# Kernel tuning notes

Measured on AMD Instinct MI355X. Metric: run time of the kernel, lower is better.

## Reference

```python
import jax, jax.numpy as jnp
import numpy as np

B, N_IN, N_OUT, K, V = 8, 2048, 2048, 64, 64


def setup_inputs() -> dict:
    key = jax.random.key(0)
    k1, k2, k3 = jax.random.split(key, 3)
    return {
        "key": jax.random.normal(k1, (B, N_IN, 1, K), dtype=jnp.float32),
        "query": jax.random.normal(k2, (B, 1, N_OUT, K), dtype=jnp.float32),
        "value": jax.random.normal(k3, (B, N_IN, V), dtype=jnp.float32),
    }


def reference(key, query, value):
    ks = key.shape[-1]
    # sum(key * query, 3) / sqrt(key_size)  ==  batched GEMM over key_size
    # weights: [B, n_inputs, n_outputs]
    weights = jnp.einsum("bik,bok->bio", key[:, :, 0, :], query[:, 0, :, :]) / jnp.sqrt(
        jnp.asarray(ks, dtype=key.dtype)
    )
    weights = jax.nn.softmax(weights, axis=1)  # softmax over n_inputs
    # sum(weights[...,None] * value[:,:,None,:], 1) -> [B, n_outputs, value_size]
    vals = jnp.einsum("bio,biv->bov", weights, value)
    # row-wise L2 normalize each [value_size] vector
    vals = vals / (jnp.linalg.norm(vals, axis=-1, keepdims=True) + 1e-12)
    values = jnp.swapaxes(vals, 1, 2)  # [B, value_size, n_outputs]
    return values, weights
```

## Files before the change

### kernel.cpp

```cpp
#include <hip/hip_runtime.h>

#define NB 8
#define NN 2048
#define KK 64
#define VV 64
#define OS 32
#define NT 32
#define SCALE 0.18033688011112043f
#define USTRIDE 36

typedef __bf16 bfrag __attribute__((ext_vector_type(8)));
typedef float  f32x4 __attribute__((ext_vector_type(4)));

__device__ __forceinline__ int swz(int row, int colByte) {
  return row * 128 + (colByte ^ ((row & 7) << 4));
}

__device__ __forceinline__ bfrag lds_frag(const unsigned short* base, int row, int colByte) {
  return *reinterpret_cast<const bfrag*>(reinterpret_cast<const char*>(base) + swz(row, colByte));
}

__device__ __forceinline__ bfrag g_frag(const float* __restrict__ g) {
  const float4* p = reinterpret_cast<const float4*>(g);
  float4 x = p[0], y = p[1];
  bfrag r;
  r[0] = (__bf16)x.x; r[1] = (__bf16)x.y; r[2] = (__bf16)x.z; r[3] = (__bf16)x.w;
  r[4] = (__bf16)y.x; r[5] = (__bf16)y.y; r[6] = (__bf16)y.z; r[7] = (__bf16)y.w;
  return r;
}

struct KS { float4 f[4]; };
__device__ __forceinline__ void k_load(KS& s, const float* __restrict__ g) {
  const float4* p = reinterpret_cast<const float4*>(g);
  s.f[0] = p[0]; s.f[1] = p[1]; s.f[2] = p[2]; s.f[3] = p[3];
}
__device__ __forceinline__ void k_write(const KS& s, unsigned short* lds, int row, int colByte) {
  const float* f = reinterpret_cast<const float*>(&s.f[0]);
  bfrag a, b;
#pragma unroll
  for (int j = 0; j < 8; ++j) a[j] = (__bf16)f[j];
#pragma unroll
  for (int j = 0; j < 8; ++j) b[j] = (__bf16)f[8 + j];
  *reinterpret_cast<bfrag*>(reinterpret_cast<char*>(lds) + swz(row, colByte)) = a;
  *reinterpret_cast<bfrag*>(reinterpret_cast<char*>(lds) + swz(row, colByte + 16)) = b;
}

struct VS { float4 f[4]; };
__device__ __forceinline__ void v_load(VS& s, const float* __restrict__ g) {
  const float4* p = reinterpret_cast<const float4*>(g);
  s.f[0] = p[0]; s.f[1] = p[1];
  const float4* q = reinterpret_cast<const float4*>(g + VV);
  s.f[2] = q[0]; s.f[3] = q[1];
}
__device__ __forceinline__ void v_write(const VS& s, unsigned short* lds, int il, int v0) {
  const float* lo = reinterpret_cast<const float*>(&s.f[0]);
  const float* hi = reinterpret_cast<const float*>(&s.f[2]);
#pragma unroll
  for (int j = 0; j < 8; ++j) {
    __bf16 two[2] = { (__bf16)lo[j], (__bf16)hi[j] };
    *reinterpret_cast<unsigned*>(reinterpret_cast<char*>(lds) + swz(v0 + j, il * 2)) =
        *reinterpret_cast<unsigned*>(two);
  }
}

__global__ void __launch_bounds__(512, 4) attn_fused(
    const float* __restrict__ key, const float* __restrict__ query,
    const float* __restrict__ value, float* __restrict__ out)
{
  __shared__ __align__(16) char smem[32768];
  __shared__ float Red[4][16];
  __shared__ float InvD[OS];
  __shared__ float Nn[OS];
  unsigned short* Kt0 = reinterpret_cast<unsigned short*>(smem);
  unsigned short* Kt1 = reinterpret_cast<unsigned short*>(smem + 8192);
  unsigned short* Vt0 = reinterpret_cast<unsigned short*>(smem + 16384);
  unsigned short* Vt1 = reinterpret_cast<unsigned short*>(smem + 24576);
  float* U0 = reinterpret_cast<float*>(smem);
  float* U1 = reinterpret_cast<float*>(smem + 9216);

  const int tid  = threadIdx.x;
  const int lane = tid & 63;
  const int w    = tid >> 6;
  const int l15  = lane & 15;
  const int l4   = lane >> 4;
  const int vhalf = w & 1;
  const int ihalf = (w >> 1) & 1;
  const int oh    = w >> 2;

  const int b  = blockIdx.x & 7;
  const int o0 = (blockIdx.x >> 3) * OS;

  const float* Kg = key   + (size_t)b * NN * KK;
  const float* Qg = query + (size_t)b * NN * KK;
  const float* Vg = value + (size_t)b * NN * VV;
  float* outV = out + (size_t)b * VV * NN;
  float* outW = out + (size_t)NB * VV * NN + (size_t)b * NN * NN;

  bfrag qb0, qb1;
  {
    const float* qr = Qg + (size_t)(o0 + oh * 16 + l15) * KK;
    qb0 = g_frag(qr + l4 * 8);
    qb1 = g_frag(qr + 32 + l4 * 8);
  }

  const int krow = tid >> 2;
  const int kel  = (tid & 3) * 16;
  const int kcb  = (tid & 3) * 32;
  const int t2   = tid & 255;
  const int vil  = (t2 & 31) * 2;
  const int vv0  = (t2 >> 5) * 8;

  KS ks; VS vs;
  if (tid < 256) { k_load(ks, Kg + (size_t)krow * KK + kel); }
  else           { v_load(vs, Vg + (size_t)vil * VV + vv0); }
  if (tid < 256) k_write(ks, Kt0, krow, kcb);
  else           v_write(vs, Vt0, vil, vv0);
  __syncthreads();

  const int ip = (l15 & 3) + ((l15 >> 2) * 8);

  f32x4 uacc[2];
  { f32x4 z = {0.f,0.f,0.f,0.f}; uacc[0] = z; uacc[1] = z; }
  float Dacc = 0.f;

  for (int t = 0; t < NT; ++t) {
    unsigned short* Kc = (t & 1) ? Kt1 : Kt0;
    unsigned short* Vc = (t & 1) ? Vt1 : Vt0;
    unsigned short* Kn = (t & 1) ? Kt0 : Kt1;
    unsigned short* Vn = (t & 1) ? Vt0 : Vt1;
    if (t + 1 < NT) {
      if (tid < 256) k_load(ks, Kg + (size_t)((t + 1) * 64 + krow) * KK + kel);
      else           v_load(vs, Vg + (size_t)((t + 1) * 64 + vil) * VV + vv0);
    }
    const int r1 = ihalf * 32 + ip;
    bfrag ka10 = lds_frag(Kc, r1,     l4 * 16);
    bfrag ka11 = lds_frag(Kc, r1,     64 + l4 * 16);
    bfrag ka20 = lds_frag(Kc, r1 + 4, l4 * 16);
    bfrag ka21 = lds_frag(Kc, r1 + 4, 64 + l4 * 16);
    f32x4 z1 = {0.f,0.f,0.f,0.f}, z2 = {0.f,0.f,0.f,0.f};
    z1 = __builtin_amdgcn_mfma_f32_16x16x32_bf16(ka10, qb0, z1, 0, 0, 0);
    z1 = __builtin_amdgcn_mfma_f32_16x16x32_bf16(ka11, qb1, z1, 0, 0, 0);
    z2 = __builtin_amdgcn_mfma_f32_16x16x32_bf16(ka20, qb0, z2, 0, 0, 0);
    z2 = __builtin_amdgcn_mfma_f32_16x16x32_bf16(ka21, qb1, z2, 0, 0, 0);
    f32x4 e1, e2;
#pragma unroll
    for (int r = 0; r < 4; ++r) e1[r] = exp2f(z1[r] * SCALE);
#pragma unroll
    for (int r = 0; r < 4; ++r) e2[r] = exp2f(z2[r] * SCALE);
    Dacc += e1[0] + e1[1] + e1[2] + e1[3] + e2[0] + e2[1] + e2[2] + e2[3];
    bfrag eb;
#pragma unroll
    for (int r = 0; r < 4; ++r) eb[r]     = (__bf16)e1[r];
#pragma unroll
    for (int r = 0; r < 4; ++r) eb[4 + r] = (__bf16)e2[r];
#pragma unroll
    for (int vg = 0; vg < 2; ++vg) {
      bfrag va = lds_frag(Vc, vhalf * 32 + vg * 16 + l15, ihalf * 64 + l4 * 16);
      uacc[vg] = __builtin_amdgcn_mfma_f32_16x16x32_bf16(va, eb, uacc[vg], 0, 0, 0);
    }
    if (t + 1 < NT) {
      if (tid < 256) k_write(ks, Kn, krow, kcb);
      else           v_write(vs, Vn, vil, vv0);
    }
    __syncthreads();
  }

  {
    float d = Dacc;
    d += __shfl_xor(d, 16, 64);
    d += __shfl_xor(d, 32, 64);
    if ((w & 1) == 0 && lane < 16) Red[w >> 1][lane] = d;
  }
  {
    float* Ur = ihalf ? U1 : U0;
#pragma unroll
    for (int vg = 0; vg < 2; ++vg)
#pragma unroll
      for (int r = 0; r < 4; ++r)
        Ur[(vhalf * 32 + vg * 16 + l4 * 4 + r) * USTRIDE + oh * 16 + l15] = uacc[vg][r];
  }
  __syncthreads();
  {
    const int v = tid >> 3, o = (tid & 7) * 4;
    f32x4 a = *reinterpret_cast<f32x4*>(&U0[v * USTRIDE + o]);
    f32x4 c = *reinterpret_cast<f32x4*>(&U1[v * USTRIDE + o]);
    a = a + c;
    *reinterpret_cast<f32x4*>(&U0[v * USTRIDE + o]) = a;
  }
  __syncthreads();
  if (tid < OS) {
    float ssq = 0.f;
#pragma unroll
    for (int v = 0; v < VV; ++v) { float x = U0[v * USTRIDE + tid]; ssq += x * x; }
    Nn[tid] = 1.f / (sqrtf(ssq) + 1e-12f);
  } else if (tid < 2 * OS) {
    const int o = tid - OS, ohh = o >> 4;
    InvD[o] = 1.f / (Red[ohh * 2][o & 15] + Red[ohh * 2 + 1][o & 15]);
  }
  __syncthreads();
  {
    const int v = tid >> 3, o = (tid & 7) * 4;
    f32x4 a  = *reinterpret_cast<f32x4*>(&U0[v * USTRIDE + o]);
    f32x4 nn = *reinterpret_cast<f32x4*>(&Nn[o]);
    f32x4 r;
#pragma unroll
    for (int j = 0; j < 4; ++j) r[j] = a[j] * nn[j];
    *reinterpret_cast<f32x4*>(&outV[(size_t)v * NN + o0 + o]) = r;
  }
  f32x4 id = *reinterpret_cast<f32x4*>(&InvD[oh * 16 + l4 * 4]);
  __syncthreads();

  const int iq    = w & 3;
  const int kbrow = tid >> 3;
  const int kseg  = tid & 7;
  {
    const float4* kp = reinterpret_cast<const float4*>(Kg + (size_t)kbrow * KK + kseg * 8);
    float4 p0 = kp[0], p1 = kp[1];
    bfrag f;
    f[0] = (__bf16)p0.x; f[1] = (__bf16)p0.y; f[2] = (__bf16)p0.z; f[3] = (__bf16)p0.w;
    f[4] = (__bf16)p1.x; f[5] = (__bf16)p1.y; f[6] = (__bf16)p1.z; f[7] = (__bf16)p1.w;
    *reinterpret_cast<bfrag*>(reinterpret_cast<char*>(Kt0) + swz(kbrow, kseg * 16)) = f;
  }
  __syncthreads();
  for (int t = 0; t < NT; ++t) {
    unsigned short* Kc = (t & 1) ? Kt1 : Kt0;
    unsigned short* Kn = (t & 1) ? Kt0 : Kt1;
    float4 p0, p1;
    if (t + 1 < NT) {
      const float4* kp = reinterpret_cast<const float4*>(
          Kg + (size_t)((t + 1) * 64 + kbrow) * KK + kseg * 8);
      p0 = kp[0]; p1 = kp[1];
    }
    bfrag kb0 = lds_frag(Kc, iq * 16 + l15, l4 * 16);
    bfrag kb1 = lds_frag(Kc, iq * 16 + l15, 64 + l4 * 16);
    f32x4 z = {0.f,0.f,0.f,0.f};
    z = __builtin_amdgcn_mfma_f32_16x16x32_bf16(qb0, kb0, z, 0, 0, 0);
    z = __builtin_amdgcn_mfma_f32_16x16x32_bf16(qb1, kb1, z, 0, 0, 0);
    f32x4 ww;
#pragma unroll
    for (int r = 0; r < 4; ++r) ww[r] = exp2f(z[r] * SCALE) * id[r];
    float* wp = outW + (size_t)(t * 64 + iq * 16 + l15) * NN + o0 + oh * 16 + l4 * 4;
    *reinterpret_cast<f32x4*>(wp) = ww;
    if (t + 1 < NT) {
      bfrag f;
      f[0] = (__bf16)p0.x; f[1] = (__bf16)p0.y; f[2] = (__bf16)p0.z; f[3] = (__bf16)p0.w;
      f[4] = (__bf16)p1.x; f[5] = (__bf16)p1.y; f[6] = (__bf16)p1.z; f[7] = (__bf16)p1.w;
      *reinterpret_cast<bfrag*>(reinterpret_cast<char*>(Kn) + swz(kbrow, kseg * 16)) = f;
    }
    __syncthreads();
  }
}

extern "C" void kernel_launch(void* const* d_in, const int* in_sizes, int n_in,
                              void* d_out, int out_size, void* d_ws, size_t ws_size,
                              hipStream_t stream) {
  (void)in_sizes; (void)n_in; (void)d_ws; (void)ws_size; (void)out_size;
  const float* key   = (const float*)d_in[0];
  const float* query = (const float*)d_in[1];
  const float* value = (const float*)d_in[2];
  float* out = (float*)d_out;
  attn_fused<<<dim3(NB * (NN / OS)), dim3(512), 0, stream>>>(key, query, value, out);
}
```

Baseline: 78.70 us.

## Double output tile to 64 columns with 1024-thread blocks and direct-global K in weight pass

Each block now covers 64 output columns with 16 waves and streams 128 input rows per step, which halves the number of blocks and halves the redundant K/V reloads. The final weight-writing pass now reads K fragments straight from global memory, with no LDS staging or barriers, and each wave produces two 16-column groups. The cross-wave reductions are reworked into a serialized accumulation over four waves and a partial sum-of-squares for the norm. This raises LDS use to 64KB per block and the register load per thread, which may reduce occupancy, and the global K reads in the final pass are less coalesced.

```diff
diff --git a/kernel.cpp b/kernel.cpp
--- a/kernel.cpp
+++ b/kernel.cpp
@@ -4,20 +4,30 @@
 #define NN 2048
 #define KK 64
 #define VV 64
-#define OS 32
-#define NT 32
+#define OS 64
+#define ITEP 128
+#define NTA (NN / ITEP)
 #define SCALE 0.18033688011112043f
-#define USTRIDE 36
+#define UST 68
 
 typedef __bf16 bfrag __attribute__((ext_vector_type(8)));
 typedef float  f32x4 __attribute__((ext_vector_type(4)));
 
-__device__ __forceinline__ int swz(int row, int colByte) {
-  return row * 128 + (colByte ^ ((row & 7) << 4));
-}
-
-__device__ __forceinline__ bfrag lds_frag(const unsigned short* base, int row, int colByte) {
-  return *reinterpret_cast<const bfrag*>(reinterpret_cast<const char*>(base) + swz(row, colByte));
+__device__ __forceinline__ int swzK(int row, int colByte) {
+  const int key = ((row & 3) << 1) | ((row >> 3) & 1);
+  return row * 128 + (colByte ^ (key << 4));
+}
+__device__ __forceinline__ int swzV(int row, int colByte) {
+  return row * 256 + (colByte ^ ((row & 7) << 4));
+}
+
+__device__ __forceinline__ bfrag kfrag(const unsigned short* base, int row, int colByte) {
+  return *reinterpret_cast<const bfrag*>(
+      reinterpret_cast<const char*>(base) + swzK(row, colByte));
+}
+__device__ __forceinline__ bfrag vfrag(const unsigned short* base, int row, int colByte) {
+  return *reinterpret_cast<const bfrag*>(
+      reinterpret_cast<const char*>(base) + swzV(row, colByte));
 }
 
 __device__ __forceinline__ bfrag g_frag(const float* __restrict__ g) {
@@ -41,8 +51,8 @@
   for (int j = 0; j < 8; ++j) a[j] = (__bf16)f[j];
 #pragma unroll
   for (int j = 0; j < 8; ++j) b[j] = (__bf16)f[8 + j];
-  *reinterpret_cast<bfrag*>(reinterpret_cast<char*>(lds) + swz(row, colByte)) = a;
-  *reinterpret_cast<bfrag*>(reinterpret_cast<char*>(lds) + swz(row, colByte + 16)) = b;
+  *reinterpret_cast<bfrag*>(reinterpret_cast<char*>(lds) + swzK(row, colByte)) = a;
+  *reinterpret_cast<bfrag*>(reinterpret_cast<char*>(lds) + swzK(row, colByte + 16)) = b;
 }
 
 struct VS { float4 f[4]; };
@@ -58,34 +68,33 @@
 #pragma unroll
   for (int j = 0; j < 8; ++j) {
     __bf16 two[2] = { (__bf16)lo[j], (__bf16)hi[j] };
-    *reinterpret_cast<unsigned*>(reinterpret_cast<char*>(lds) + swz(v0 + j, il * 2)) =
+    *reinterpret_cast<unsigned*>(reinterpret_cast<char*>(lds) + swzV(v0 + j, il * 2)) =
         *reinterpret_cast<unsigned*>(two);
   }
 }
 
-__global__ void __launch_bounds__(512, 4) attn_fused(
+__global__ void __launch_bounds__(1024, 4) attn_fused(
     const float* __restrict__ key, const float* __restrict__ query,
     const float* __restrict__ value, float* __restrict__ out)
 {
-  __shared__ __align__(16) char smem[32768];
-  __shared__ float Red[4][16];
+  __shared__ __align__(16) char smem[65536];
+  __shared__ float Red[16][16];
   __shared__ float InvD[OS];
   __shared__ float Nn[OS];
   unsigned short* Kt0 = reinterpret_cast<unsigned short*>(smem);
-  unsigned short* Kt1 = reinterpret_cast<unsigned short*>(smem + 8192);
-  unsigned short* Vt0 = reinterpret_cast<unsigned short*>(smem + 16384);
-  unsigned short* Vt1 = reinterpret_cast<unsigned short*>(smem + 24576);
-  float* U0 = reinterpret_cast<float*>(smem);
-  float* U1 = reinterpret_cast<float*>(smem + 9216);
+  unsigned short* Kt1 = reinterpret_cast<unsigned short*>(smem + 16384);
+  unsigned short* Vt0 = reinterpret_cast<unsigned short*>(smem + 32768);
+  unsigned short* Vt1 = reinterpret_cast<unsigned short*>(smem + 49152);
+  float* Ured = reinterpret_cast<float*>(smem);
+  float* R2   = reinterpret_cast<float*>(smem + 20480);
 
   const int tid  = threadIdx.x;
   const int lane = tid & 63;
   const int w    = tid >> 6;
   const int l15  = lane & 15;
   const int l4   = lane >> 4;
-  const int vhalf = w & 1;
-  const int ihalf = (w >> 1) & 1;
-  const int oh    = w >> 2;
+  const int oh   = w >> 2;
+  const int iq   = w & 3;
 
   const int b  = blockIdx.x & 7;
   const int o0 = (blockIdx.x >> 3) * OS;
@@ -106,37 +115,39 @@
   const int krow = tid >> 2;
   const int kel  = (tid & 3) * 16;
   const int kcb  = (tid & 3) * 32;
-  const int t2   = tid & 255;
-  const int vil  = (t2 & 31) * 2;
-  const int vv0  = (t2 >> 5) * 8;
+  const int t2   = tid - 512;
+  const int vil  = (t2 & 63) * 2;
+  const int vg8  = (t2 >> 6) & 7;
+  const int vv0  = vg8 * 8;
 
   KS ks; VS vs;
-  if (tid < 256) { k_load(ks, Kg + (size_t)krow * KK + kel); }
+  if (tid < 512) { k_load(ks, Kg + (size_t)krow * KK + kel); }
   else           { v_load(vs, Vg + (size_t)vil * VV + vv0); }
-  if (tid < 256) k_write(ks, Kt0, krow, kcb);
+  if (tid < 512) k_write(ks, Kt0, krow, kcb);
   else           v_write(vs, Vt0, vil, vv0);
   __syncthreads();
 
   const int ip = (l15 & 3) + ((l15 >> 2) * 8);
 
-  f32x4 uacc[2];
-  { f32x4 z = {0.f,0.f,0.f,0.f}; uacc[0] = z; uacc[1] = z; }
+  f32x4 uacc[4];
+#pragma unroll
+  for (int vg = 0; vg < 4; ++vg) { f32x4 z = {0.f,0.f,0.f,0.f}; uacc[vg] = z; }
   float Dacc = 0.f;
 
-  for (int t = 0; t < NT; ++t) {
+  for (int t = 0; t < NTA; ++t) {
     unsigned short* Kc = (t & 1) ? Kt1 : Kt0;
     unsigned short* Vc = (t & 1) ? Vt1 : Vt0;
     unsigned short* Kn = (t & 1) ? Kt0 : Kt1;
     unsigned short* Vn = (t & 1) ? Vt0 : Vt1;
-    if (t + 1 < NT) {
-      if (tid < 256) k_load(ks, Kg + (size_t)((t + 1) * 64 + krow) * KK + kel);
-      else           v_load(vs, Vg + (size_t)((t + 1) * 64 + vil) * VV + vv0);
-    }
-    const int r1 = ihalf * 32 + ip;
-    bfrag ka10 = lds_frag(Kc, r1,     l4 * 16);
-    bfrag ka11 = lds_frag(Kc, r1,     64 + l4 * 16);
-    bfrag ka20 = lds_frag(Kc, r1 + 4, l4 * 16);
-    bfrag ka21 = lds_frag(Kc, r1 + 4, 64 + l4 * 16);
+    if (t + 1 < NTA) {
+      if (tid < 512) k_load(ks, Kg + (size_t)((t + 1) * ITEP + krow) * KK + kel);
+      else           v_load(vs, Vg + (size_t)((t + 1) * ITEP + vil) * VV + vv0);
+    }
+    const int r1 = iq * 32 + ip;
+    bfrag ka10 = kfrag(Kc, r1,     l4 * 16);
+    bfrag ka11 = kfrag(Kc, r1,     64 + l4 * 16);
+    bfrag ka20 = kfrag(Kc, r1 + 4, l4 * 16);
+    bfrag ka21 = kfrag(Kc, r1 + 4, 64 + l4 * 16);
     f32x4 z1 = {0.f,0.f,0.f,0.f}, z2 = {0.f,0.f,0.f,0.f};
     z1 = __builtin_amdgcn_mfma_f32_16x16x32_bf16(ka10, qb0, z1, 0, 0, 0);
     z1 = __builtin_amdgcn_mfma_f32_16x16x32_bf16(ka11, qb1, z1, 0, 0, 0);
@@ -154,12 +165,12 @@
 #pragma unroll
     for (int r = 0; r < 4; ++r) eb[4 + r] = (__bf16)e2[r];
 #pragma unroll
-    for (int vg = 0; vg < 2; ++vg) {
-      bfrag va = lds_frag(Vc, vhalf * 32 + vg * 16 + l15, ihalf * 64 + l4 * 16);
+    for (int vg = 0; vg < 4; ++vg) {
+      bfrag va = vfrag(Vc, vg * 16 + l15, iq * 64 + l4 * 16);
       uacc[vg] = __builtin_amdgcn_mfma_f32_16x16x32_bf16(va, eb, uacc[vg], 0, 0, 0);
     }
-    if (t + 1 < NT) {
-      if (tid < 256) k_write(ks, Kn, krow, kcb);
+    if (t + 1 < NTA) {
+      if (tid < 512) k_write(ks, Kn, krow, kcb);
       else           v_write(vs, Vn, vil, vv0);
     }
     __syncthreads();
@@ -169,85 +180,83 @@
     float d = Dacc;
     d += __shfl_xor(d, 16, 64);
     d += __shfl_xor(d, 32, 64);
-    if ((w & 1) == 0 && lane < 16) Red[w >> 1][lane] = d;
-  }
-  {
-    float* Ur = ihalf ? U1 : U0;
-#pragma unroll
-    for (int vg = 0; vg < 2; ++vg)
-#pragma unroll
-      for (int r = 0; r < 4; ++r)
-        Ur[(vhalf * 32 + vg * 16 + l4 * 4 + r) * USTRIDE + oh * 16 + l15] = uacc[vg][r];
-  }
-  __syncthreads();
-  {
-    const int v = tid >> 3, o = (tid & 7) * 4;
-    f32x4 a = *reinterpret_cast<f32x4*>(&U0[v * USTRIDE + o]);
-    f32x4 c = *reinterpret_cast<f32x4*>(&U1[v * USTRIDE + o]);
-    a = a + c;
-    *reinterpret_cast<f32x4*>(&U0[v * USTRIDE + o]) = a;
+    if (lane < 16) Red[w][lane] = d;
+  }
+#pragma unroll
+  for (int q = 0; q < 4; ++q) {
+    if (iq == q) {
+#pragma unroll
+      for (int vg = 0; vg < 4; ++vg)
+#pragma unroll
+        for (int r = 0; r < 4; ++r) {
+          const int idx = (vg * 16 + l4 * 4 + r) * UST + oh * 16 + l15;
+          if (q == 0) Ured[idx] = uacc[vg][r];
+          else        Ured[idx] += uacc[vg][r];
+        }
+    }
+    __syncthreads();
+  }
+  {
+    const int vgr = tid >> 6;
+    const int o   = tid & 63;
+    float s = 0.f;
+#pragma unroll
+    for (int j = 0; j < 4; ++j) {
+      float x = Ured[(vgr * 4 + j) * UST + o];
+      s += x * x;
+    }
+    R2[vgr * 64 + o] = s;
   }
   __syncthreads();
   if (tid < OS) {
-    float ssq = 0.f;
-#pragma unroll
-    for (int v = 0; v < VV; ++v) { float x = U0[v * USTRIDE + tid]; ssq += x * x; }
-    Nn[tid] = 1.f / (sqrtf(ssq) + 1e-12f);
+    float n = 0.f;
+#pragma unroll
+    for (int g = 0; g < 16; ++g) n += R2[g * 64 + tid];
+    Nn[tid] = 1.f / (sqrtf(n) + 1e-12f);
   } else if (tid < 2 * OS) {
-    const int o = tid - OS, ohh = o >> 4;
-    InvD[o] = 1.f / (Red[ohh * 2][o & 15] + Red[ohh * 2 + 1][o & 15]);
+    const int o = tid - OS;
+    const int ohh = o >> 4;
+    InvD[o] = 1.f / (Red[ohh * 4 + 0][o & 15] + Red[ohh * 4 + 1][o & 15] +
+                     Red[ohh * 4 + 2][o & 15] + Red[ohh * 4 + 3][o & 15]);
   }
   __syncthreads();
   {
-    const int v = tid >> 3, o = (tid & 7) * 4;
-    f32x4 a  = *reinterpret_cast<f32x4*>(&U0[v * USTRIDE + o]);
-    f32x4 nn = *reinterpret_cast<f32x4*>(&Nn[o]);
+    const int v  = tid >> 4;
+    const int og = (tid & 15) * 4;
+    f32x4 u = *reinterpret_cast<f32x4*>(&Ured[v * UST + og]);
     f32x4 r;
 #pragma unroll
-    for (int j = 0; j < 4; ++j) r[j] = a[j] * nn[j];
-    *reinterpret_cast<f32x4*>(&outV[(size_t)v * NN + o0 + o]) = r;
-  }
-  f32x4 id = *reinterpret_cast<f32x4*>(&InvD[oh * 16 + l4 * 4]);
-  __syncthreads();
-
-  const int iq    = w & 3;
-  const int kbrow = tid >> 3;
-  const int kseg  = tid & 7;
-  {
-    const float4* kp = reinterpret_cast<const float4*>(Kg + (size_t)kbrow * KK + kseg * 8);
-    float4 p0 = kp[0], p1 = kp[1];
-    bfrag f;
-    f[0] = (__bf16)p0.x; f[1] = (__bf16)p0.y; f[2] = (__bf16)p0.z; f[3] = (__bf16)p0.w;
-    f[4] = (__bf16)p1.x; f[5] = (__bf16)p1.y; f[6] = (__bf16)p1.z; f[7] = (__bf16)p1.w;
-    *reinterpret_cast<bfrag*>(reinterpret_cast<char*>(Kt0) + swz(kbrow, kseg * 16)) = f;
-  }
-  __syncthreads();
-  for (int t = 0; t < NT; ++t) {
-    unsigned short* Kc = (t & 1) ? Kt1 : Kt0;
-    unsigned short* Kn = (t & 1) ? Kt0 : Kt1;
-    float4 p0, p1;
-    if (t + 1 < NT) {
-      const float4* kp = reinterpret_cast<const float4*>(
-          Kg + (size_t)((t + 1) * 64 + kbrow) * KK + kseg * 8);
-      p0 = kp[0]; p1 = kp[1];
-    }
-    bfrag kb0 = lds_frag(Kc, iq * 16 + l15, l4 * 16);
-    bfrag kb1 = lds_frag(Kc, iq * 16 + l15, 64 + l4 * 16);
-    f32x4 z = {0.f,0.f,0.f,0.f};
-    z = __builtin_amdgcn_mfma_f32_16x16x32_bf16(qb0, kb0, z, 0, 0, 0);
-    z = __builtin_amdgcn_mfma_f32_16x16x32_bf16(qb1, kb1, z, 0, 0, 0);
-    f32x4 ww;
-#pragma unroll
-    for (int r = 0; r < 4; ++r) ww[r] = exp2f(z[r] * SCALE) * id[r];
-    float* wp = outW + (size_t)(t * 64 + iq * 16 + l15) * NN + o0 + oh * 16 + l4 * 4;
-    *reinterpret_cast<f32x4*>(wp) = ww;
-    if (t + 1 < NT) {
-      bfrag f;
-      f[0] = (__bf16)p0.x; f[1] = (__bf16)p0.y; f[2] = (__bf16)p0.z; f[3] = (__bf16)p0.w;
-      f[4] = (__bf16)p1.x; f[5] = (__bf16)p1.y; f[6] = (__bf16)p1.z; f[7] = (__bf16)p1.w;
-      *reinterpret_cast<bfrag*>(reinterpret_cast<char*>(Kn) + swz(kbrow, kseg * 16)) = f;
-    }
-    __syncthreads();
+    for (int j = 0; j < 4; ++j) r[j] = u[j] * Nn[og + j];
+    *reinterpret_cast<f32x4*>(&outV[(size_t)v * NN + o0 + og]) = r;
+  }
+
+  const int ohf = w & 1;
+  const int ic  = w >> 1;
+  bfrag qA[2][2];
+  f32x4 id[2];
+#pragma unroll
+  for (int g = 0; g < 2; ++g) {
+    const float* qr = Qg + (size_t)(o0 + ohf * 32 + g * 16 + l15) * KK;
+    qA[g][0] = g_frag(qr + l4 * 8);
+    qA[g][1] = g_frag(qr + 32 + l4 * 8);
+    id[g] = *reinterpret_cast<const f32x4*>(&InvD[ohf * 32 + g * 16 + l4 * 4]);
+  }
+  for (int t = 0; t < 16; ++t) {
+    const int ibase = ic * 256 + t * 16;
+    const float* kr = Kg + (size_t)(ibase + l15) * KK;
+    bfrag kb0 = g_frag(kr + l4 * 8);
+    bfrag kb1 = g_frag(kr + 32 + l4 * 8);
+#pragma unroll
+    for (int g = 0; g < 2; ++g) {
+      f32x4 z = {0.f,0.f,0.f,0.f};
+      z = __builtin_amdgcn_mfma_f32_16x16x32_bf16(qA[g][0], kb0, z, 0, 0, 0);
+      z = __builtin_amdgcn_mfma_f32_16x16x32_bf16(qA[g][1], kb1, z, 0, 0, 0);
+      f32x4 ww;
+#pragma unroll
+      for (int r = 0; r < 4; ++r) ww[r] = exp2f(z[r] * SCALE) * id[g][r];
+      float* wp = outW + (size_t)(ibase + l15) * NN + o0 + ohf * 32 + g * 16 + l4 * 4;
+      *reinterpret_cast<f32x4*>(wp) = ww;
+    }
   }
 }
 
@@ -259,5 +268,5 @@
   const float* query = (const float*)d_in[1];
   const float* value = (const float*)d_in[2];
   float* out = (float*)d_out;
-  attn_fused<<<dim3(NB * (NN / OS)), dim3(512), 0, stream>>>(key, query, value, out);
-}
+  attn_fused<<<dim3(NB * (NN / OS)), dim3(1024), 0, stream>>>(key, query, value, out);
+}
```

After: 78.68 us. Within noise of the previous version (-0.0%).
